# Kernel tuning notes

Hardware: AMD Instinct MI355X
Metric: run time of the kernel (lower is better)

The kernel has to match this reference:

```python
import jax, jax.numpy as jnp
import numpy as np

EPS = 1e-5
TOP_K = 2


def setup_inputs() -> dict:
    key = jax.random.key(0)
    ks = jax.random.split(key, 6)
    T, H, F, E = 4096, 1024, 2816, 8
    scale = 0.02
    return {
        "hidden_states": jax.random.normal(ks[0], (T, H), dtype=jnp.float32),
        "ln_w": jnp.ones((H,), dtype=jnp.float32),
        "router_w": jax.random.normal(ks[1], (H, E), dtype=jnp.float32) * scale,
        "w_gate": jax.random.normal(ks[2], (E, H, F), dtype=jnp.float32) * scale,
        "w_up": jax.random.normal(ks[3], (E, H, F), dtype=jnp.float32) * scale,
        "w_down": jax.random.normal(ks[4], (E, F, H), dtype=jnp.float32) * scale,
    }


def reference(hidden_states, ln_w, router_w, w_gate, w_up, w_down):
    # RMSNorm (LlamaRMSNorm)
    var = jnp.mean(hidden_states * hidden_states, axis=-1, keepdims=True)
    x = hidden_states * jax.lax.rsqrt(var + EPS) * ln_w  # [T, H]

    # TopKRouter: softmax over experts, then top-k probs/indices
    logits = x @ router_w                     # [T, E]
    probs = jax.nn.softmax(logits, axis=-1)
    topk_p, topk_i = jax.lax.top_k(probs, TOP_K)  # [T, K]

    # Dense combine weights [T, E]: prob for routed experts, 0 otherwise
    T = x.shape[0]
    combine = jnp.zeros_like(probs).at[jnp.arange(T)[:, None], topk_i].add(topk_p)

    # Experts: Llama-style gated MLP (SwiGLU); loop over fixed small expert set
    out = jnp.zeros_like(x)
    for e in range(w_gate.shape[0]):
        h = jax.nn.silu(x @ w_gate[e]) * (x @ w_up[e])   # [T, F]
        out = out + combine[:, e:e + 1] * (h @ w_down[e])
    return out
```

## Files before the change

### kernel.cpp

```cpp
#include <hip/hip_runtime.h>

#define T_TOK 4096
#define H_DIM 1024
#define F_DIM 2816
#define E_NUM 8
#define EPSV 1e-5f
#define MAX_TILES 72

typedef unsigned short u16;
typedef __attribute__((ext_vector_type(8))) short bf16x8;
typedef __attribute__((ext_vector_type(4))) float f32x4;

__device__ __forceinline__ u16 f2bf(float f) {
  union { float f; unsigned u; } c; c.f = f;
  unsigned u = c.u;
  return (u16)((u + 0x7FFFu + ((u >> 16) & 1u)) >> 16);
}

__device__ __forceinline__ void llds16(const u16* g, u16* l) {
  __builtin_amdgcn_global_load_lds(
      (const __attribute__((address_space(1))) unsigned int*)g,
      (__attribute__((address_space(3))) unsigned int*)l, 16, 0, 0);
}

__global__ __launch_bounds__(256) void router_kernel(
    const float* __restrict__ hs, const float* __restrict__ lnw,
    const float* __restrict__ rw, u16* __restrict__ x_h,
    int* __restrict__ cnt, int* __restrict__ list,
    float* __restrict__ wcomb, int* __restrict__ slot) {
  const int wave = threadIdx.x >> 6;
  const int lane = threadIdx.x & 63;
  const int t = blockIdx.x * 4 + wave;
  const float* row = hs + (size_t)t * H_DIM;

  float4 v[4];
  float ss = 0.f;
#pragma unroll
  for (int j = 0; j < 4; ++j) {
    v[j] = ((const float4*)row)[j * 64 + lane];
    ss += v[j].x * v[j].x + v[j].y * v[j].y + v[j].z * v[j].z + v[j].w * v[j].w;
  }
#pragma unroll
  for (int m = 32; m; m >>= 1) ss += __shfl_xor(ss, m, 64);
  const float inv = rsqrtf(ss * (1.0f / H_DIM) + EPSV);

  float lg[E_NUM];
#pragma unroll
  for (int e = 0; e < E_NUM; ++e) lg[e] = 0.f;

#pragma unroll
  for (int j = 0; j < 4; ++j) {
    const int idx = j * 64 + lane;
    const int h0 = idx * 4;
    float4 w4 = ((const float4*)lnw)[idx];
    float xv[4] = {v[j].x * inv * w4.x, v[j].y * inv * w4.y,
                   v[j].z * inv * w4.z, v[j].w * inv * w4.w};
    ushort4 xs;
    xs.x = f2bf(xv[0]); xs.y = f2bf(xv[1]); xs.z = f2bf(xv[2]); xs.w = f2bf(xv[3]);
    ((ushort4*)(x_h + (size_t)t * H_DIM))[idx] = xs;
#pragma unroll
    for (int q = 0; q < 4; ++q) {
      const float* rr = rw + (size_t)(h0 + q) * E_NUM;
      float4 a = ((const float4*)rr)[0];
      float4 b = ((const float4*)rr)[1];
      lg[0] += xv[q] * a.x; lg[1] += xv[q] * a.y;
      lg[2] += xv[q] * a.z; lg[3] += xv[q] * a.w;
      lg[4] += xv[q] * b.x; lg[5] += xv[q] * b.y;
      lg[6] += xv[q] * b.z; lg[7] += xv[q] * b.w;
    }
  }
#pragma unroll
  for (int e = 0; e < E_NUM; ++e)
#pragma unroll
    for (int m = 32; m; m >>= 1) lg[e] += __shfl_xor(lg[e], m, 64);

  if (lane == 0) {
    float mx = lg[0];
#pragma unroll
    for (int e = 1; e < E_NUM; ++e) mx = fmaxf(mx, lg[e]);
    float p[E_NUM], s = 0.f;
#pragma unroll
    for (int e = 0; e < E_NUM; ++e) { p[e] = __expf(lg[e] - mx); s += p[e]; }
    const float invs = 1.0f / s;
    int e1 = 0; float b1 = p[0];
#pragma unroll
    for (int e = 1; e < E_NUM; ++e) if (p[e] > b1) { b1 = p[e]; e1 = e; }
    int e2 = -1; float b2 = -1.f;
#pragma unroll
    for (int e = 0; e < E_NUM; ++e) if (e != e1 && p[e] > b2) { b2 = p[e]; e2 = e; }
    b1 *= invs; b2 *= invs;
    int p1 = atomicAdd(&cnt[e1], 1);
    list[e1 * T_TOK + p1] = t; wcomb[e1 * T_TOK + p1] = b1;
    slot[2 * t] = (e1 << 16) | p1;
    int p2 = atomicAdd(&cnt[e2], 1);
    list[e2 * T_TOK + p2] = t; wcomb[e2 * T_TOK + p2] = b2;
    slot[2 * t + 1] = (e2 << 16) | p2;
  }
}

__global__ void offsets_kernel(const int* __restrict__ cnt, int* __restrict__ offs,
                               int* __restrict__ tmap) {
  if (threadIdx.x == 0) {
    int s = 0, ty = 0;
    for (int e = 0; e < E_NUM; ++e) {
      offs[e] = s; s += cnt[e];
      const int nt = (cnt[e] + 127) >> 7;
      for (int r = 0; r < nt; ++r) tmap[ty++] = (e << 16) | r;
    }
    for (; ty < MAX_TILES; ++ty) tmap[ty] = -1;
  }
}

#define TPW 5632
__global__ __launch_bounds__(256) void transpose_cvt_all(
    const float* __restrict__ wg, const float* __restrict__ wu,
    const float* __restrict__ wd, u16* __restrict__ wgT,
    u16* __restrict__ wuT, u16* __restrict__ wdT) {
  __shared__ float tile[128][37];
  const int bx = blockIdx.x;
  const int which = bx / TPW;
  const int rem = bx - which * TPW;
  const int e = rem / 704;
  const int t = rem - e * 704;
  const float* in; u16* outp; int R, C, rt, ct;
  if (which == 0)      { in = wg; outp = wgT; R = H_DIM; C = F_DIM; rt = t / 88; ct = t - rt * 88; }
  else if (which == 1) { in = wu; outp = wuT; R = H_DIM; C = F_DIM; rt = t / 88; ct = t - rt * 88; }
  else                 { in = wd; outp = wdT; R = F_DIM; C = H_DIM; rt = t >> 5; ct = t & 31; }
  const size_t base = (size_t)e * R * C;
  const int r0 = rt * 128, c0 = ct * 32;
  const int tid = threadIdx.x;

  const int rr = tid >> 3, cq = tid & 7;
#pragma unroll
  for (int i = 0; i < 4; ++i) {
    float4 v = *(const float4*)(in + base + (size_t)(r0 + rr + 32 * i) * C + c0 + cq * 4);
    float* dst = &tile[rr + 32 * i][cq * 4];
    dst[0] = v.x; dst[1] = v.y; dst[2] = v.z; dst[3] = v.w;
  }
  __syncthreads();

  const int cc = tid >> 4, rq0 = tid & 15;
#pragma unroll
  for (int jj = 0; jj < 4; ++jj) {
    const int c = cc + 16 * (jj & 1);
    const int rq = rq0 + 16 * (jj >> 1);
    ushort4 o;
    o.x = f2bf(tile[rq * 4 + 0][c]);
    o.y = f2bf(tile[rq * 4 + 1][c]);
    o.z = f2bf(tile[rq * 4 + 2][c]);
    o.w = f2bf(tile[rq * 4 + 3][c]);
    *(ushort4*)(outp + base + (size_t)(c0 + c) * R + r0 + rq * 4) = o;
  }
}

__global__ __launch_bounds__(256, 4) void gemm1_kernel(
    const u16* __restrict__ x_h, const u16* __restrict__ wgT,
    const u16* __restrict__ wuT, const int* __restrict__ cnt,
    const int* __restrict__ offs, const int* __restrict__ list,
    const int* __restrict__ tmap, u16* __restrict__ hbuf) {
  const int tme = tmap[blockIdx.y];
  if (tme < 0) return;
  const int e = tme >> 16, rt = tme & 0xFFFF;
  const int n_e = cnt[e];
  const int ft = blockIdx.x;

  __shared__ __align__(16) u16 As[128 * 64];
  __shared__ __align__(16) u16 Bgs[64 * 64];
  __shared__ __align__(16) u16 Bus[64 * 64];

  const int tid = threadIdx.x;
  const int wv = tid >> 6, lane = tid & 63;
  const int wm = wv >> 1, wn = wv & 1;
  const int lrow = lane & 15, quad = lane >> 4;
  const int srow = lane >> 3, schunk = lane & 7;

  const u16* agp[4];
#pragma unroll
  for (int i = 0; i < 4; ++i) {
    const int rl = wv * 32 + i * 8 + srow;
    int gr = rt * 128 + rl; if (gr >= n_e) gr = n_e - 1;
    const int tkn = list[e * T_TOK + gr];
    agp[i] = x_h + (size_t)tkn * H_DIM + ((schunk ^ (rl & 7)) << 3);
  }
  const size_t wb = ((size_t)e * F_DIM + (size_t)ft * 64) * H_DIM;
  const u16* bgp[2]; const u16* bup[2];
#pragma unroll
  for (int i = 0; i < 2; ++i) {
    const int r = wv * 16 + i * 8 + srow;
    const size_t g = wb + (size_t)r * H_DIM + ((schunk ^ (r & 7)) << 3);
    bgp[i] = wgT + g;
    bup[i] = wuT + g;
  }

  int aoff[4][2], boff[2][2];
#pragma unroll
  for (int tm = 0; tm < 4; ++tm) {
    const int row = wm * 64 + tm * 16 + lrow;
#pragma unroll
    for (int ks = 0; ks < 2; ++ks)
      aoff[tm][ks] = row * 64 + (((ks * 4 + quad) ^ (row & 7)) << 3);
  }
#pragma unroll
  for (int tn = 0; tn < 2; ++tn) {
    const int row = wn * 32 + tn * 16 + lrow;
#pragma unroll
    for (int ks = 0; ks < 2; ++ks)
      boff[tn][ks] = row * 64 + (((ks * 4 + quad) ^ (row & 7)) << 3);
  }

  f32x4 accg[4][2], accu[4][2];
#pragma unroll
  for (int i = 0; i < 4; ++i)
#pragma unroll
    for (int j = 0; j < 2; ++j) {
      accg[i][j] = f32x4{0.f, 0.f, 0.f, 0.f};
      accu[i][j] = f32x4{0.f, 0.f, 0.f, 0.f};
    }

#pragma unroll 1
  for (int k0 = 0; k0 < H_DIM; k0 += 64) {
#pragma unroll
    for (int i = 0; i < 4; ++i)
      llds16(agp[i] + k0, &As[(wv * 32 + i * 8) * 64]);
#pragma unroll
    for (int i = 0; i < 2; ++i) {
      llds16(bgp[i] + k0, &Bgs[(wv * 16 + i * 8) * 64]);
      llds16(bup[i] + k0, &Bus[(wv * 16 + i * 8) * 64]);
    }
    __syncthreads();
#pragma unroll
    for (int ks = 0; ks < 2; ++ks) {
      bf16x8 a[4], bg[2], bu[2];
#pragma unroll
      for (int tm = 0; tm < 4; ++tm) a[tm] = *(const bf16x8*)&As[aoff[tm][ks]];
#pragma unroll
      for (int tn = 0; tn < 2; ++tn) {
        bg[tn] = *(const bf16x8*)&Bgs[boff[tn][ks]];
        bu[tn] = *(const bf16x8*)&Bus[boff[tn][ks]];
      }
#pragma unroll
      for (int tm = 0; tm < 4; ++tm)
#pragma unroll
        for (int tn = 0; tn < 2; ++tn) {
          accg[tm][tn] = __builtin_amdgcn_mfma_f32_16x16x32_bf16(a[tm], bg[tn], accg[tm][tn], 0, 0, 0);
          accu[tm][tn] = __builtin_amdgcn_mfma_f32_16x16x32_bf16(a[tm], bu[tn], accu[tm][tn], 0, 0, 0);
        }
    }
    __syncthreads();
  }

  const int oe = offs[e];
#pragma unroll
  for (int tm = 0; tm < 4; ++tm) {
    const int lr0 = wm * 64 + tm * 16 + quad * 4;
#pragma unroll
    for (int rr = 0; rr < 4; ++rr) {
      const int gr = rt * 128 + lr0 + rr;
      if (gr < n_e) {
#pragma unroll
        for (int tn = 0; tn < 2; ++tn) {
          float g = accg[tm][tn][rr];
          float u = accu[tm][tn][rr];
          float hv = g / (1.0f + __expf(-g)) * u;
          int col = ft * 64 + wn * 32 + tn * 16 + lrow;
          hbuf[(size_t)(oe + gr) * F_DIM + col] = f2bf(hv);
        }
      }
    }
  }
}

__global__ __launch_bounds__(256, 4) void gemm2_kernel(
    const u16* __restrict__ hbuf, const u16* __restrict__ wdT,
    const int* __restrict__ cnt, const int* __restrict__ offs,
    const float* __restrict__ wcomb, const int* __restrict__ tmap,
    float* __restrict__ contrib) {
  const int tme = tmap[blockIdx.y];
  if (tme < 0) return;
  const int e = tme >> 16, rt = tme & 0xFFFF;
  const int n_e = cnt[e];
  const int nt = blockIdx.x;

  __shared__ __align__(16) u16 As[128 * 64];
  __shared__ __align__(16) u16 Bs[128 * 64];

  const int tid = threadIdx.x;
  const int oe = offs[e];
  const int wv = tid >> 6, lane = tid & 63;
  const int wm = wv >> 1, wn = wv & 1;
  const int lrow = lane & 15, quad = lane >> 4;
  const int srow = lane >> 3, schunk = lane & 7;

  const u16* agp[4];
#pragma unroll
  for (int i = 0; i < 4; ++i) {
    const int rl = wv * 32 + i * 8 + srow;
    int gr = rt * 128 + rl; if (gr >= n_e) gr = n_e - 1;
    agp[i] = hbuf + (size_t)(oe + gr) * F_DIM + ((schunk ^ (rl & 7)) << 3);
  }
  const size_t wb = ((size_t)e * H_DIM + (size_t)nt * 128) * F_DIM;
  const u16* bgp[4];
#pragma unroll
  for (int i = 0; i < 4; ++i) {
    const int r = wv * 32 + i * 8 + srow;
    bgp[i] = wdT + wb + (size_t)r * F_DIM + ((schunk ^ (r & 7)) << 3);
  }

  int aoff[4][2], boff[4][2];
#pragma unroll
  for (int tm = 0; tm < 4; ++tm) {
    const int row = wm * 64 + tm * 16 + lrow;
#pragma unroll
    for (int ks = 0; ks < 2; ++ks)
      aoff[tm][ks] = row * 64 + (((ks * 4 + quad) ^ (row & 7)) << 3);
  }
#pragma unroll
  for (int tn = 0; tn < 4; ++tn) {
    const int row = wn * 64 + tn * 16 + lrow;
#pragma unroll
    for (int ks = 0; ks < 2; ++ks)
      boff[tn][ks] = row * 64 + (((ks * 4 + quad) ^ (row & 7)) << 3);
  }

  f32x4 acc[4][4];
#pragma unroll
  for (int i = 0; i < 4; ++i)
#pragma unroll
    for (int j = 0; j < 4; ++j) acc[i][j] = f32x4{0.f, 0.f, 0.f, 0.f};

#pragma unroll 1
  for (int k0 = 0; k0 < F_DIM; k0 += 64) {
#pragma unroll
    for (int i = 0; i < 4; ++i) {
      llds16(agp[i] + k0, &As[(wv * 32 + i * 8) * 64]);
      llds16(bgp[i] + k0, &Bs[(wv * 32 + i * 8) * 64]);
    }
    __syncthreads();
#pragma unroll
    for (int ks = 0; ks < 2; ++ks) {
      bf16x8 a[4], bb[4];
#pragma unroll
      for (int tm = 0; tm < 4; ++tm) a[tm] = *(const bf16x8*)&As[aoff[tm][ks]];
#pragma unroll
      for (int tn = 0; tn < 4; ++tn) bb[tn] = *(const bf16x8*)&Bs[boff[tn][ks]];
#pragma unroll
      for (int tm = 0; tm < 4; ++tm)
#pragma unroll
        for (int tn = 0; tn < 4; ++tn)
          acc[tm][tn] = __builtin_amdgcn_mfma_f32_16x16x32_bf16(a[tm], bb[tn], acc[tm][tn], 0, 0, 0);
    }
    __syncthreads();
  }

#pragma unroll
  for (int tm = 0; tm < 4; ++tm) {
    const int lr0 = wm * 64 + tm * 16 + quad * 4;
#pragma unroll
    for (int rr = 0; rr < 4; ++rr) {
      const int gr = rt * 128 + lr0 + rr;
      if (gr < n_e) {
        const float cw = wcomb[e * T_TOK + gr];
#pragma unroll
        for (int tn = 0; tn < 4; ++tn) {
          const int col = nt * 128 + wn * 64 + tn * 16 + lrow;
          contrib[(size_t)(oe + gr) * H_DIM + col] = acc[tm][tn][rr] * cw;
        }
      }
    }
  }
}

__global__ __launch_bounds__(256) void combine_kernel(
    const float* __restrict__ contrib, const int* __restrict__ offs,
    const int* __restrict__ slot, float* __restrict__ out) {
  const int t = blockIdx.x;
  const int s0 = slot[2 * t], s1 = slot[2 * t + 1];
  const int r0 = offs[s0 >> 16] + (s0 & 0xFFFF);
  const int r1 = offs[s1 >> 16] + (s1 & 0xFFFF);
  float4 a = ((const float4*)(contrib + (size_t)r0 * H_DIM))[threadIdx.x];
  float4 b = ((const float4*)(contrib + (size_t)r1 * H_DIM))[threadIdx.x];
  float4 o = {a.x + b.x, a.y + b.y, a.z + b.z, a.w + b.w};
  ((float4*)(out + (size_t)t * H_DIM))[threadIdx.x] = o;
}

extern "C" void kernel_launch(void* const* d_in, const int* in_sizes, int n_in,
                              void* d_out, int out_size, void* d_ws, size_t ws_size,
                              hipStream_t stream) {
  const float* hs  = (const float*)d_in[0];
  const float* lnw = (const float*)d_in[1];
  const float* rw  = (const float*)d_in[2];
  const float* wg  = (const float*)d_in[3];
  const float* wu  = (const float*)d_in[4];
  const float* wd  = (const float*)d_in[5];
  float* out = (float*)d_out;

  char* p = (char*)d_ws;
  const size_t SZ_XH = (size_t)T_TOK * H_DIM * 2;
  const size_t SZ_W  = (size_t)E_NUM * F_DIM * H_DIM * 2;
  const size_t SZ_HB = (size_t)T_TOK * 2 * F_DIM * 2;
  const size_t SZ_CT = (size_t)T_TOK * 2 * H_DIM * 4;

  u16* x_h  = (u16*)p;   p += SZ_XH;
  u16* wgT  = (u16*)p;   p += SZ_W;
  u16* wuT  = (u16*)p;   p += SZ_W;
  u16* wdT  = (u16*)p;   p += SZ_W;
  u16* hbuf = (u16*)p;   p += SZ_HB;
  float* contrib = (float*)p; p += SZ_CT;
  int* cnt  = (int*)p;   p += 256;
  int* offs = (int*)p;   p += 256;
  int* tmap = (int*)p;   p += 512;
  int* list = (int*)p;   p += (size_t)E_NUM * T_TOK * 4;
  float* wcomb = (float*)p; p += (size_t)E_NUM * T_TOK * 4;
  int* slot = (int*)p;   p += (size_t)T_TOK * 2 * 4;

  hipMemsetAsync(cnt, 0, 256, stream);
  router_kernel<<<T_TOK / 4, 256, 0, stream>>>(hs, lnw, rw, x_h, cnt, list, wcomb, slot);
  offsets_kernel<<<1, 64, 0, stream>>>(cnt, offs, tmap);
  transpose_cvt_all<<<3 * TPW, 256, 0, stream>>>(wg, wu, wd, wgT, wuT, wdT);
  gemm1_kernel<<<dim3(F_DIM / 64, MAX_TILES), 256, 0, stream>>>(x_h, wgT, wuT, cnt, offs, list, tmap, hbuf);
  gemm2_kernel<<<dim3(H_DIM / 128, MAX_TILES), 256, 0, stream>>>(hbuf, wdT, cnt, offs, wcomb, tmap, contrib);
  combine_kernel<<<T_TOK, 256, 0, stream>>>(contrib, offs, slot, out);
}
```

Before: 588.1 us.

## Fold offsets into transpose kernel, widen transpose tiles, halve gemm2 N-tile

Removes the single-thread offsets kernel launch by having block 0 of the transpose kernel compute offsets and the tile map. The transpose now handles 128x64 tiles with batched float4 loads and 16-byte bf16 stores, cutting the block count and using wider writes. gemm2 switches from a 128-wide to a 64-wide N tile, doubling its grid so more blocks are available to fill the CUs. The cost is less B reuse per block and more redundant reads of the A tile.

```diff
diff --git a/kernel.cpp b/kernel.cpp
--- a/kernel.cpp
+++ b/kernel.cpp
@@ -9,6 +9,7 @@
 
 typedef unsigned short u16;
 typedef __attribute__((ext_vector_type(8))) short bf16x8;
+typedef __attribute__((ext_vector_type(8))) unsigned short u16x8;
 typedef __attribute__((ext_vector_type(4))) float f32x4;
 
 __device__ __forceinline__ u16 f2bf(float f) {
@@ -98,9 +99,14 @@
   }
 }
 
-__global__ void offsets_kernel(const int* __restrict__ cnt, int* __restrict__ offs,
-                               int* __restrict__ tmap) {
-  if (threadIdx.x == 0) {
+#define TPW2 2816
+__global__ __launch_bounds__(256) void transpose_cvt_all(
+    const float* __restrict__ wg, const float* __restrict__ wu,
+    const float* __restrict__ wd, u16* __restrict__ wgT,
+    u16* __restrict__ wuT, u16* __restrict__ wdT,
+    const int* __restrict__ cnt, int* __restrict__ offs,
+    int* __restrict__ tmap) {
+  if (blockIdx.x == 0 && threadIdx.x == 0) {
     int s = 0, ty = 0;
     for (int e = 0; e < E_NUM; ++e) {
       offs[e] = s; s += cnt[e];
@@ -109,47 +115,43 @@
     }
     for (; ty < MAX_TILES; ++ty) tmap[ty] = -1;
   }
-}
-
-#define TPW 5632
-__global__ __launch_bounds__(256) void transpose_cvt_all(
-    const float* __restrict__ wg, const float* __restrict__ wu,
-    const float* __restrict__ wd, u16* __restrict__ wgT,
-    u16* __restrict__ wuT, u16* __restrict__ wdT) {
-  __shared__ float tile[128][37];
+
+  __shared__ float tile[128][65];
   const int bx = blockIdx.x;
-  const int which = bx / TPW;
-  const int rem = bx - which * TPW;
-  const int e = rem / 704;
-  const int t = rem - e * 704;
+  const int which = bx / TPW2;
+  const int rem = bx - which * TPW2;
+  const int e = rem / 352;
+  const int t = rem - e * 352;
   const float* in; u16* outp; int R, C, rt, ct;
-  if (which == 0)      { in = wg; outp = wgT; R = H_DIM; C = F_DIM; rt = t / 88; ct = t - rt * 88; }
-  else if (which == 1) { in = wu; outp = wuT; R = H_DIM; C = F_DIM; rt = t / 88; ct = t - rt * 88; }
-  else                 { in = wd; outp = wdT; R = F_DIM; C = H_DIM; rt = t >> 5; ct = t & 31; }
+  if (which == 0)      { in = wg; outp = wgT; R = H_DIM; C = F_DIM; rt = t / 44; ct = t - rt * 44; }
+  else if (which == 1) { in = wu; outp = wuT; R = H_DIM; C = F_DIM; rt = t / 44; ct = t - rt * 44; }
+  else                 { in = wd; outp = wdT; R = F_DIM; C = H_DIM; rt = t >> 4; ct = t & 15; }
   const size_t base = (size_t)e * R * C;
-  const int r0 = rt * 128, c0 = ct * 32;
+  const int r0 = rt * 128, c0 = ct * 64;
   const int tid = threadIdx.x;
 
-  const int rr = tid >> 3, cq = tid & 7;
-#pragma unroll
-  for (int i = 0; i < 4; ++i) {
-    float4 v = *(const float4*)(in + base + (size_t)(r0 + rr + 32 * i) * C + c0 + cq * 4);
-    float* dst = &tile[rr + 32 * i][cq * 4];
-    dst[0] = v.x; dst[1] = v.y; dst[2] = v.z; dst[3] = v.w;
+  const int rrow = tid >> 4, chunk = tid & 15;
+  float4 v[8];
+#pragma unroll
+  for (int it = 0; it < 8; ++it) {
+    const int r = it * 16 + rrow;
+    v[it] = *(const float4*)(in + base + (size_t)(r0 + r) * C + c0 + chunk * 4);
+  }
+#pragma unroll
+  for (int it = 0; it < 8; ++it) {
+    float* dst = &tile[it * 16 + rrow][chunk * 4];
+    dst[0] = v[it].x; dst[1] = v[it].y; dst[2] = v[it].z; dst[3] = v[it].w;
   }
   __syncthreads();
 
-  const int cc = tid >> 4, rq0 = tid & 15;
-#pragma unroll
-  for (int jj = 0; jj < 4; ++jj) {
-    const int c = cc + 16 * (jj & 1);
-    const int rq = rq0 + 16 * (jj >> 1);
-    ushort4 o;
-    o.x = f2bf(tile[rq * 4 + 0][c]);
-    o.y = f2bf(tile[rq * 4 + 1][c]);
-    o.z = f2bf(tile[rq * 4 + 2][c]);
-    o.w = f2bf(tile[rq * 4 + 3][c]);
-    *(ushort4*)(outp + base + (size_t)(c0 + c) * R + r0 + rq * 4) = o;
+  const int cc = tid >> 4, rq = tid & 15;
+#pragma unroll
+  for (int it = 0; it < 4; ++it) {
+    const int c = it * 16 + cc;
+    u16x8 o;
+#pragma unroll
+    for (int j = 0; j < 8; ++j) o[j] = f2bf(tile[rq * 8 + j][c]);
+    *(u16x8*)(outp + base + (size_t)(c0 + c) * R + r0 + rq * 8) = o;
   }
 }
 
@@ -282,7 +284,7 @@
   const int nt = blockIdx.x;
 
   __shared__ __align__(16) u16 As[128 * 64];
-  __shared__ __align__(16) u16 Bs[128 * 64];
+  __shared__ __align__(16) u16 Bs[64 * 64];
 
   const int tid = threadIdx.x;
   const int oe = offs[e];
@@ -298,15 +300,15 @@
     int gr = rt * 128 + rl; if (gr >= n_e) gr = n_e - 1;
     agp[i] = hbuf + (size_t)(oe + gr) * F_DIM + ((schunk ^ (rl & 7)) << 3);
   }
-  const size_t wb = ((size_t)e * H_DIM + (size_t)nt * 128) * F_DIM;
-  const u16* bgp[4];
-#pragma unroll
-  for (int i = 0; i < 4; ++i) {
-    const int r = wv * 32 + i * 8 + srow;
+  const size_t wb = ((size_t)e * H_DIM + (size_t)nt * 64) * F_DIM;
+  const u16* bgp[2];
+#pragma unroll
+  for (int i = 0; i < 2; ++i) {
+    const int r = wv * 16 + i * 8 + srow;
     bgp[i] = wdT + wb + (size_t)r * F_DIM + ((schunk ^ (r & 7)) << 3);
   }
 
-  int aoff[4][2], boff[4][2];
+  int aoff[4][2], boff[2][2];
 #pragma unroll
   for (int tm = 0; tm < 4; ++tm) {
     const int row = wm * 64 + tm * 16 + lrow;
@@ -315,38 +317,39 @@
       aoff[tm][ks] = row * 64 + (((ks * 4 + quad) ^ (row & 7)) << 3);
   }
 #pragma unroll
-  for (int tn = 0; tn < 4; ++tn) {
-    const int row = wn * 64 + tn * 16 + lrow;
+  for (int tn = 0; tn < 2; ++tn) {
+    const int row = wn * 32 + tn * 16 + lrow;
 #pragma unroll
     for (int ks = 0; ks < 2; ++ks)
       boff[tn][ks] = row * 64 + (((ks * 4 + quad) ^ (row & 7)) << 3);
   }
 
-  f32x4 acc[4][4];
+  f32x4 acc[4][2];
 #pragma unroll
   for (int i = 0; i < 4; ++i)
 #pragma unroll
-    for (int j = 0; j < 4; ++j) acc[i][j] = f32x4{0.f, 0.f, 0.f, 0.f};
+    for (int j = 0; j < 2; ++j) acc[i][j] = f32x4{0.f, 0.f, 0.f, 0.f};
 
 #pragma unroll 1
   for (int k0 = 0; k0 < F_DIM; k0 += 64) {
 #pragma unroll
-    for (int i = 0; i < 4; ++i) {
+    for (int i = 0; i < 4; ++i)
       llds16(agp[i] + k0, &As[(wv * 32 + i * 8) * 64]);
-      llds16(bgp[i] + k0, &Bs[(wv * 32 + i * 8) * 64]);
-    }
+#pragma unroll
+    for (int i = 0; i < 2; ++i)
+      llds16(bgp[i] + k0, &Bs[(wv * 16 + i * 8) * 64]);
     __syncthreads();
 #pragma unroll
     for (int ks = 0; ks < 2; ++ks) {
-      bf16x8 a[4], bb[4];
+      bf16x8 a[4], bb[2];
 #pragma unroll
       for (int tm = 0; tm < 4; ++tm) a[tm] = *(const bf16x8*)&As[aoff[tm][ks]];
 #pragma unroll
-      for (int tn = 0; tn < 4; ++tn) bb[tn] = *(const bf16x8*)&Bs[boff[tn][ks]];
+      for (int tn = 0; tn < 2; ++tn) bb[tn] = *(const bf16x8*)&Bs[boff[tn][ks]];
 #pragma unroll
       for (int tm = 0; tm < 4; ++tm)
 #pragma unroll
-        for (int tn = 0; tn < 4; ++tn)
+        for (int tn = 0; tn < 2; ++tn)
           acc[tm][tn] = __builtin_amdgcn_mfma_f32_16x16x32_bf16(a[tm], bb[tn], acc[tm][tn], 0, 0, 0);
     }
     __syncthreads();
@@ -361,8 +364,8 @@
       if (gr < n_e) {
         const float cw = wcomb[e * T_TOK + gr];
 #pragma unroll
-        for (int tn = 0; tn < 4; ++tn) {
-          const int col = nt * 128 + wn * 64 + tn * 16 + lrow;
+        for (int tn = 0; tn < 2; ++tn) {
+          const int col = nt * 64 + wn * 32 + tn * 16 + lrow;
           contrib[(size_t)(oe + gr) * H_DIM + col] = acc[tm][tn][rr] * cw;
         }
       }
@@ -415,9 +418,8 @@
 
   hipMemsetAsync(cnt, 0, 256, stream);
   router_kernel<<<T_TOK / 4, 256, 0, stream>>>(hs, lnw, rw, x_h, cnt, list, wcomb, slot);
-  offsets_kernel<<<1, 64, 0, stream>>>(cnt, offs, tmap);
-  transpose_cvt_all<<<3 * TPW, 256, 0, stream>>>(wg, wu, wd, wgT, wuT, wdT);
+  transpose_cvt_all<<<3 * TPW2, 256, 0, stream>>>(wg, wu, wd, wgT, wuT, wdT, cnt, offs, tmap);
   gemm1_kernel<<<dim3(F_DIM / 64, MAX_TILES), 256, 0, stream>>>(x_h, wgT, wuT, cnt, offs, list, tmap, hbuf);
-  gemm2_kernel<<<dim3(H_DIM / 128, MAX_TILES), 256, 0, stream>>>(hbuf, wdT, cnt, offs, wcomb, tmap, contrib);
+  gemm2_kernel<<<dim3(H_DIM / 64, MAX_TILES), 256, 0, stream>>>(hbuf, wdT, cnt, offs, wcomb, tmap, contrib);
   combine_kernel<<<T_TOK, 256, 0, stream>>>(contrib, offs, slot, out);
 }
```

Result: no change. 587.8 us (-0.0%).
